# Performance work log

Measured on AMD Instinct MI355X. Metric: run time of the kernel, lower is better.

## Reference

```python
import jax, jax.numpy as jnp
import numpy as np

N = 50000      # nodes
E = 800000     # edges
D = 300        # emb_dim
G = 256        # graphs in batch
OUT = 128      # out_channels
NUM_BOND_TYPE = 6       # includes self-loop type id 4
NUM_BOND_DIR = 3
SELF_LOOP_TYPE = 4


def setup_inputs() -> dict:
    key = jax.random.key(0)
    ks = jax.random.split(key, 12)
    s = 0.05
    x = jax.random.normal(ks[0], (N, D), jnp.float32)
    edge_index = jax.random.randint(ks[1], (2, E), 0, N, dtype=jnp.int32)
    edge_attr = jax.random.randint(ks[2], (E, 2), 0, NUM_BOND_DIR, dtype=jnp.int32)
    batch = jnp.sort(jax.random.randint(ks[3], (N,), 0, G, dtype=jnp.int32))
    # 5 stacked GINConv layers: MLP(D->2D->D) + two edge-embedding tables each
    W1 = jax.random.normal(ks[4], (5, D, 2 * D), jnp.float32) * s
    b1 = jnp.zeros((5, 2 * D), jnp.float32)
    W2 = jax.random.normal(ks[5], (5, 2 * D, D), jnp.float32) * s
    b2 = jnp.zeros((5, D), jnp.float32)
    ee1 = jax.random.normal(ks[6], (5, NUM_BOND_TYPE, D), jnp.float32) * s
    ee2 = jax.random.normal(ks[7], (5, NUM_BOND_DIR, D), jnp.float32) * s
    lin1_W = jax.random.normal(ks[8], (D, D // 2), jnp.float32) * s
    lin1_b = jnp.zeros((D // 2,), jnp.float32)
    lin2_W = jax.random.normal(ks[9], (D // 2, OUT), jnp.float32) * s
    lin2_b = jnp.zeros((OUT,), jnp.float32)
    return dict(x=x, W1=W1, b1=b1, W2=W2, b2=b2, ee1=ee1, ee2=ee2,
                lin1_W=lin1_W, lin1_b=lin1_b, lin2_W=lin2_W, lin2_b=lin2_b,
                edge_index=edge_index, edge_attr=edge_attr, batch=batch)


def _gin_conv(x, edge_index, edge_attr, W1, b1, W2, b2, ee1, ee2):
    src, dst = edge_index[0], edge_index[1]
    e = ee1[edge_attr[:, 0]] + ee2[edge_attr[:, 1]]          # [E, D]
    msg = x[src] + e                                          # gather + edge-add
    agg = jax.ops.segment_sum(msg, dst, num_segments=x.shape[0])  # scatter-sum
    # self loops with edge_attr (SELF_LOOP_TYPE, 0): contributes x_i + ee1[4] + ee2[0]
    agg = agg + x + ee1[SELF_LOOP_TYPE] + ee2[0]
    h = jnp.maximum(agg @ W1 + b1, 0.0) @ W2 + b2             # MLP(D->2D->D)
    return h


def reference(x, W1, b1, W2, b2, ee1, ee2, lin1_W, lin1_b, lin2_W, lin2_b,
              edge_index, edge_attr, batch):
    h = x
    for l in range(5):
        h = _gin_conv(h, edge_index, edge_attr,
                      W1[l], b1[l], W2[l], b2[l], ee1[l], ee2[l])
    # global_add_pool over graphs
    g = jax.ops.segment_sum(h, batch, num_segments=G)          # [G, D]
    g = jnp.maximum(g @ lin1_W + lin1_b, 0.0)                  # dropout is identity in eval
    out = g @ lin2_W + lin2_b                                  # [G, OUT]
    return out
```

## Files before the change

### kernel.cpp

```cpp
#include <hip/hip_runtime.h>
#include <hip/hip_bf16.h>

#define NN 50000
#define EE 800000
#define DD 300
#define GG 256
#define RS  320
#define RSU 80

#define NK1 10
#define NT1 40
#define NK2 19
#define NT2 24
#define PACK1 ((size_t)NT1 * NK1 * 512)
#define PACK2 ((size_t)NT2 * NK2 * 512)
#define HSTR 1216

#define SCB 49

typedef short bf16x8 __attribute__((ext_vector_type(8)));
typedef float f32x4  __attribute__((ext_vector_type(4)));

__device__ inline unsigned short f2bf(float f) {
    unsigned u = __float_as_uint(f);
    return (unsigned short)((u + 0x7fffu + ((u >> 16) & 1u)) >> 16);
}
__device__ inline unsigned pk2(float a, float b) {
    return (unsigned)f2bf(a) | ((unsigned)f2bf(b) << 16);
}
__device__ inline void acc8(float* a, uint4 v) {
    a[0] += __uint_as_float(v.x << 16); a[1] += __uint_as_float(v.x & 0xffff0000u);
    a[2] += __uint_as_float(v.y << 16); a[3] += __uint_as_float(v.y & 0xffff0000u);
    a[4] += __uint_as_float(v.z << 16); a[5] += __uint_as_float(v.z & 0xffff0000u);
    a[6] += __uint_as_float(v.w << 16); a[7] += __uint_as_float(v.w & 0xffff0000u);
}
__device__ inline int deg3(int p) {
    return (p & 1023) + ((p >> 10) & 1023) + ((p >> 20) & 1023);
}

__global__ __launch_bounds__(256)
void count_kernel(const int* __restrict__ ei, const int* __restrict__ ea,
                  int* __restrict__ cnt1p, int* __restrict__ cnt2p)
{
    int e = blockIdx.x * 256 + threadIdx.x;
    if (e >= EE) return;
    int dst = ei[EE + e];
    int a0  = ea[e * 2];
    int a1  = ea[e * 2 + 1];
    atomicAdd(&cnt1p[dst], 1 << (10 * a0));
    atomicAdd(&cnt2p[dst], 1 << (10 * a1));
}

__global__ __launch_bounds__(256)
void scan1_kernel(const int* __restrict__ cnt1p, int* __restrict__ blocksum)
{
    __shared__ int ws[4];
    int tid = threadIdx.x;
    int n0 = blockIdx.x * 1024 + tid * 4;
    int s = 0;
#pragma unroll
    for (int i = 0; i < 4; ++i) {
        int n = n0 + i;
        if (n < NN) s += deg3(cnt1p[n]);
    }
    for (int off = 1; off < 64; off <<= 1) s += __shfl_xor(s, off);
    if ((tid & 63) == 0) ws[tid >> 6] = s;
    __syncthreads();
    if (tid == 0) blocksum[blockIdx.x] = ws[0] + ws[1] + ws[2] + ws[3];
}

__global__ __launch_bounds__(256)
void scan2_kernel(const int* __restrict__ cnt1p, const int* __restrict__ blocksum,
                  int* __restrict__ rowptr, int* __restrict__ cursor)
{
    __shared__ int ws[4];
    __shared__ int boff;
    int tid = threadIdx.x;
    int b   = blockIdx.x;
    if (tid < 64) {
        int v = (tid < b) ? blocksum[tid] : 0;
        for (int off = 1; off < 64; off <<= 1) v += __shfl_xor(v, off);
        if (tid == 0) boff = v;
    }
    int n0 = b * 1024 + tid * 4;
    int d[4]; int s = 0;
#pragma unroll
    for (int i = 0; i < 4; ++i) {
        int n = n0 + i;
        d[i] = (n < NN) ? deg3(cnt1p[n]) : 0;
        s += d[i];
    }
    int lane = tid & 63, w = tid >> 6;
    int inc = s;
    for (int off = 1; off < 64; off <<= 1) {
        int t = __shfl_up(inc, off);
        if (lane >= off) inc += t;
    }
    if (lane == 63) ws[w] = inc;
    __syncthreads();
    int woff = 0;
#pragma unroll
    for (int i = 0; i < 4; ++i) if (i < w) woff += ws[i];
    int excl = boff + woff + inc - s;
#pragma unroll
    for (int i = 0; i < 4; ++i) {
        int n = n0 + i;
        if (n < NN) { rowptr[n] = excl; cursor[n] = excl; }
        excl += d[i];
    }
    if (b == SCB - 1 && tid == 255) rowptr[NN] = EE;
}

__global__ __launch_bounds__(256)
void fill_kernel(const int* __restrict__ ei, int* __restrict__ cursor,
                 int* __restrict__ csr_src)
{
    int e = blockIdx.x * 256 + threadIdx.x;
    if (e >= EE) return;
    int dst = ei[EE + e];
    int src = ei[e];
    int pos = atomicAdd(&cursor[dst], 1);
    csr_src[pos] = src;
}

__global__ __launch_bounds__(256)
void pack_all(const float* __restrict__ W1, const float* __restrict__ W2,
              short* __restrict__ W1p, short* __restrict__ W2p)
{
    const int TL = NT1 * NK1 + NT2 * NK2;
    int idx = blockIdx.x * 256 + threadIdx.x;
    if (idx >= 5 * TL * 64) return;
    int lane  = idx & 63;
    int tile  = idx >> 6;
    int layer = tile / TL;
    int tl    = tile - layer * TL;
    const float* W; short* outp;
    int K, N, nt_i, kt, pos;
    if (tl < NT1 * NK1) {
        nt_i = tl / NK1; kt = tl % NK1;
        W = W1 + (size_t)layer * DD * 600;
        outp = W1p + layer * PACK1;
        K = 300; N = 600;
        pos = kt * NT1 + nt_i;
    } else {
        tl -= NT1 * NK1;
        nt_i = tl / NK2; kt = tl % NK2;
        W = W2 + (size_t)layer * 600 * DD;
        outp = W2p + layer * PACK2;
        K = 600; N = 300;
        pos = kt * NT2 + nt_i;
    }
    int col = nt_i * 16 + (lane & 15);
    int k0  = kt * 32 + (lane >> 4) * 8;
    unsigned short v[8];
#pragma unroll
    for (int j = 0; j < 8; ++j) {
        int r = k0 + j;
        float f = (r < K && col < N) ? W[(size_t)r * N + col] : 0.0f;
        v[j] = f2bf(f);
    }
    uint4 p;
    p.x = (unsigned)v[0] | ((unsigned)v[1] << 16);
    p.y = (unsigned)v[2] | ((unsigned)v[3] << 16);
    p.z = (unsigned)v[4] | ((unsigned)v[5] << 16);
    p.w = (unsigned)v[6] | ((unsigned)v[7] << 16);
    ((uint4*)outp)[(size_t)pos * 64 + lane] = p;
}

__global__ __launch_bounds__(256)
void init_kernel(const float* __restrict__ x, short* __restrict__ Xbf,
                 short* __restrict__ Ybf)
{
    int i = blockIdx.x * 256 + threadIdx.x;
    const int TX = NN * RSU;
    if (i < TX) {
        int row = i / RSU, pu = i - row * RSU;
        uint2 o = make_uint2(0u, 0u);
        if (pu < 75) {
            float4 v = ((const float4*)x)[row * 75 + pu];
            o = make_uint2(pk2(v.x, v.y), pk2(v.z, v.w));
        }
        ((uint2*)Xbf)[i] = o;
    } else {
        int j = i - TX;
        if (j < (NN + 64) * 5) {
            int row = j / 5, pu = 75 + (j - row * 5);
            ((uint2*)Ybf)[(size_t)row * RSU + pu] = make_uint2(0u, 0u);
        }
    }
}

__global__ __launch_bounds__(256)
void agg_gather(const short* __restrict__ Hbf, const int* __restrict__ rowptr,
                const int* __restrict__ csr_src, const int* __restrict__ cnt1p,
                const int* __restrict__ cnt2p, const float* __restrict__ ee1l,
                const float* __restrict__ ee2l, short* __restrict__ outbf)
{
    int n    = blockIdx.x * 4 + (threadIdx.x >> 6);
    int lane = threadIdx.x & 63;
    if (n >= NN || lane >= 40) return;
    const uint4* HU = (const uint4*)Hbf;
    const int cb = lane * 8;

    float aA[8], aB[8], aC[8], aD[8];
#pragma unroll
    for (int k = 0; k < 8; ++k) { aA[k] = 0.f; aB[k] = 0.f; aC[k] = 0.f; aD[k] = 0.f; }

    int p1 = cnt1p[n], p2 = cnt2p[n];
    float c10 = (float)(p1 & 1023), c11 = (float)((p1 >> 10) & 1023),
          c12 = (float)((p1 >> 20) & 1023);
    float c20 = (float)(p2 & 1023), c21 = (float)((p2 >> 10) & 1023),
          c22 = (float)((p2 >> 20) & 1023);

#define EEADD(rowp, s)                                                        \
    {                                                                         \
        if (lane <= 36) {                                                     \
            float4 v0 = *(const float4*)((rowp) + cb);                        \
            float4 v1 = *(const float4*)((rowp) + cb + 4);                    \
            aA[0] = fmaf(v0.x, (s), aA[0]); aA[1] = fmaf(v0.y, (s), aA[1]);   \
            aA[2] = fmaf(v0.z, (s), aA[2]); aA[3] = fmaf(v0.w, (s), aA[3]);   \
            aA[4] = fmaf(v1.x, (s), aA[4]); aA[5] = fmaf(v1.y, (s), aA[5]);   \
            aA[6] = fmaf(v1.z, (s), aA[6]); aA[7] = fmaf(v1.w, (s), aA[7]);   \
        } else if (lane == 37) {                                              \
            float4 v0 = *(const float4*)((rowp) + cb);                        \
            aA[0] = fmaf(v0.x, (s), aA[0]); aA[1] = fmaf(v0.y, (s), aA[1]);   \
            aA[2] = fmaf(v0.z, (s), aA[2]); aA[3] = fmaf(v0.w, (s), aA[3]);   \
        }                                                                     \
    }
    EEADD(ee1l + 4 * 300, 1.0f);
    EEADD(ee1l, c10); EEADD(ee1l + 300, c11); EEADD(ee1l + 600, c12);
    EEADD(ee2l, c20 + 1.0f);
    EEADD(ee2l + 300, c21); EEADD(ee2l + 600, c22);
#undef EEADD

    acc8(aB, HU[(size_t)n * 40 + lane]);

    int e   = rowptr[n];
    int end = rowptr[n + 1];
    for (; e + 4 <= end; e += 4) {
        uint4 v0 = HU[(size_t)csr_src[e]     * 40 + lane];
        uint4 v1 = HU[(size_t)csr_src[e + 1] * 40 + lane];
        uint4 v2 = HU[(size_t)csr_src[e + 2] * 40 + lane];
        uint4 v3 = HU[(size_t)csr_src[e + 3] * 40 + lane];
        acc8(aA, v0); acc8(aB, v1); acc8(aC, v2); acc8(aD, v3);
    }
    for (; e < end; ++e) acc8(aA, HU[(size_t)csr_src[e] * 40 + lane]);

    uint4 o;
    o.x = pk2(aA[0] + aB[0] + aC[0] + aD[0], aA[1] + aB[1] + aC[1] + aD[1]);
    o.y = pk2(aA[2] + aB[2] + aC[2] + aD[2], aA[3] + aB[3] + aC[3] + aD[3]);
    o.z = pk2(aA[4] + aB[4] + aC[4] + aD[4], aA[5] + aB[5] + aC[5] + aD[5]);
    o.w = pk2(aA[6] + aB[6] + aC[6] + aD[6], aA[7] + aB[7] + aC[7] + aD[7]);
    ((uint4*)(outbf + (size_t)n * RS))[lane] = o;
}

__global__ __launch_bounds__(512, 3)
void mlp_mfma(const short* __restrict__ Ybf, const short* __restrict__ W1p,
              const float* __restrict__ b1, const short* __restrict__ W2p,
              const float* __restrict__ b2, short* __restrict__ Xbf, int nrows)
{
    __shared__ __align__(16) short Hs[32 * 608];
    char* HsB = (char*)Hs;
    const int tid  = threadIdx.x;
    const int ch   = tid >> 6;
    const int lane = tid & 63;
    const int row0 = blockIdx.x * 32;
    const int l15  = lane & 15;
    const int q    = lane >> 4;
    const int hr   = q * 4;

    const short* A0 = Ybf + (size_t)(row0 + l15) * RS;
    const short* A1 = A0 + 16 * RS;
    const char* W1B = (const char*)W1p + (ch * 5) * 1024 + lane * 16;
    const char* W2B = (const char*)W2p + (ch * 3) * 1024 + lane * 16;

    f32x4 acc[5][2];
#pragma unroll
    for (int t = 0; t < 5; ++t) {
        acc[t][0] = (f32x4){0.f, 0.f, 0.f, 0.f};
        acc[t][1] = (f32x4){0.f, 0.f, 0.f, 0.f};
    }
    bf16x8 aa[3][2], bb[3][5];
#pragma unroll
    for (int p = 0; p < 2; ++p) {
        aa[p][0] = *(const bf16x8*)&A0[p * 32 + q * 8];
        aa[p][1] = *(const bf16x8*)&A1[p * 32 + q * 8];
        const char* src = W1B + p * (NT1 * 1024);
#pragma unroll
        for (int t = 0; t < 5; ++t) bb[p][t] = *(const bf16x8*)(src + t * 1024);
    }
#pragma unroll
    for (int kt = 0; kt < NK1; ++kt) {
        const int cur = kt % 3;
        if (kt + 2 < NK1) {
            const int nx = (kt + 2) % 3;
            aa[nx][0] = *(const bf16x8*)&A0[(kt + 2) * 32 + q * 8];
            aa[nx][1] = *(const bf16x8*)&A1[(kt + 2) * 32 + q * 8];
            const char* src = W1B + (kt + 2) * (NT1 * 1024);
#pragma unroll
            for (int t = 0; t < 5; ++t) bb[nx][t] = *(const bf16x8*)(src + t * 1024);
        }
#pragma unroll
        for (int t = 0; t < 5; ++t) {
            acc[t][0] = __builtin_amdgcn_mfma_f32_16x16x32_bf16(aa[cur][0], bb[cur][t], acc[t][0], 0, 0, 0);
            acc[t][1] = __builtin_amdgcn_mfma_f32_16x16x32_bf16(aa[cur][1], bb[cur][t], acc[t][1], 0, 0, 0);
        }
    }

    bf16x8 bfr[3][3];
#pragma unroll
    for (int p = 0; p < 2; ++p) {
        const char* src = W2B + p * (NT2 * 1024);
#pragma unroll
        for (int t = 0; t < 3; ++t) bfr[p][t] = *(const bf16x8*)(src + t * 1024);
    }

#pragma unroll
    for (int t = 0; t < 5; ++t) {
        int col = (ch * 5 + t) * 16 + l15;
        if (col < 608) {
            float bbv = col < 600 ? b1[col] : 0.0f;
#pragma unroll
            for (int m = 0; m < 2; ++m)
#pragma unroll
                for (int j = 0; j < 4; ++j) {
                    int row = m * 16 + hr + j;
                    float v = acc[t][m][j] + bbv;
                    v = v > 0.0f ? v : 0.0f;
                    int bo = 2 * col;
                    int boS = (bo < 1152) ? (bo ^ ((row & 7) << 4)) : bo;
                    *(short*)(HsB + row * HSTR + boS) = (short)f2bf(v);
                }
        }
    }
    __syncthreads();

    f32x4 acc2[3][2];
#pragma unroll
    for (int t = 0; t < 3; ++t) {
        acc2[t][0] = (f32x4){0.f, 0.f, 0.f, 0.f};
        acc2[t][1] = (f32x4){0.f, 0.f, 0.f, 0.f};
    }
    const int r0 = l15;
    const int r1 = r0 + 16;
    const int swz = (r0 & 7) << 4;
    bf16x8 hh[3][2];
#pragma unroll
    for (int p = 0; p < 2; ++p) {
        int bo  = p * 64 + q * 16;
        int boS = (bo < 1152) ? (bo ^ swz) : bo;
        hh[p][0] = *(const bf16x8*)(HsB + r0 * HSTR + boS);
        hh[p][1] = *(const bf16x8*)(HsB + r1 * HSTR + boS);
    }
#pragma unroll
    for (int kt = 0; kt < NK2; ++kt) {
        const int cur = kt % 3;
        if (kt + 2 < NK2) {
            const int nx = (kt + 2) % 3;
            const char* src = W2B + (kt + 2) * (NT2 * 1024);
#pragma unroll
            for (int t = 0; t < 3; ++t) bfr[nx][t] = *(const bf16x8*)(src + t * 1024);
            int bo  = (kt + 2) * 64 + q * 16;
            int boS = (bo < 1152) ? (bo ^ swz) : bo;
            hh[nx][0] = *(const bf16x8*)(HsB + r0 * HSTR + boS);
            hh[nx][1] = *(const bf16x8*)(HsB + r1 * HSTR + boS);
        }
#pragma unroll
        for (int t = 0; t < 3; ++t) {
            acc2[t][0] = __builtin_amdgcn_mfma_f32_16x16x32_bf16(hh[cur][0], bfr[cur][t], acc2[t][0], 0, 0, 0);
            acc2[t][1] = __builtin_amdgcn_mfma_f32_16x16x32_bf16(hh[cur][1], bfr[cur][t], acc2[t][1], 0, 0, 0);
        }
    }
#pragma unroll
    for (int t = 0; t < 3; ++t) {
        int col = (ch * 3 + t) * 16 + l15;
        if (col < 300) {
            float bbv = b2[col];
#pragma unroll
            for (int m = 0; m < 2; ++m)
#pragma unroll
                for (int j = 0; j < 4; ++j) {
                    int gr = row0 + m * 16 + hr + j;
                    if (gr < nrows)
                        Xbf[(size_t)gr * RS + col] = (short)f2bf(acc2[t][m][j] + bbv);
                }
        }
    }
}

__global__ __launch_bounds__(160)
void pool_kernel(const short* __restrict__ Xbf, const int* __restrict__ batch,
                 float* __restrict__ g)
{
    int tid = threadIdx.x;
    if (tid >= 150) return;
    int n0 = blockIdx.x * 64;
    int n1 = n0 + 64; if (n1 > NN) n1 = NN;
    int nlast = n1 - 1;
    float s0 = 0.0f, s1 = 0.0f;
    int cur = batch[n0];
    unsigned v = *(const unsigned*)&Xbf[(size_t)n0 * RS + tid * 2];
    for (int n = n0; n < n1; ++n) {
        int np = n + 1; np = np > nlast ? nlast : np;
        unsigned vnext = *(const unsigned*)&Xbf[(size_t)np * RS + tid * 2];
        int b = batch[n];
        if (b != cur) {
            atomicAdd(&g[cur * DD + tid * 2], s0);
            atomicAdd(&g[cur * DD + tid * 2 + 1], s1);
            s0 = 0.0f; s1 = 0.0f; cur = b;
        }
        s0 += __uint_as_float(v << 16);
        s1 += __uint_as_float(v & 0xffff0000u);
        v = vnext;
    }
    atomicAdd(&g[cur * DD + tid * 2], s0);
    atomicAdd(&g[cur * DD + tid * 2 + 1], s1);
}

__global__ __launch_bounds__(160)
void head_kernel(const float* __restrict__ g, const float* __restrict__ l1W,
                 const float* __restrict__ l1b, const float* __restrict__ l2W,
                 const float* __restrict__ l2b, float* __restrict__ out)
{
    __shared__ float g2s[152];
    int r = blockIdx.x, tid = threadIdx.x;
    const float* gr = g + r * DD;
    if (tid < 150) {
        float acc = 0.0f;
        for (int k = 0; k < DD; ++k) acc = fmaf(gr[k], l1W[k * 150 + tid], acc);
        acc += l1b[tid];
        g2s[tid] = acc > 0.0f ? acc : 0.0f;
    }
    __syncthreads();
    if (tid < 128) {
        float acc = 0.0f;
        for (int k = 0; k < 150; ++k) acc = fmaf(g2s[k], l2W[k * 128 + tid], acc);
        out[r * 128 + tid] = acc + l2b[tid];
    }
}

extern "C" void kernel_launch(void* const* d_in, const int* in_sizes, int n_in,
                              void* d_out, int out_size, void* d_ws, size_t ws_size,
                              hipStream_t stream)
{
    const float* x     = (const float*)d_in[0];
    const float* W1    = (const float*)d_in[1];
    const float* b1    = (const float*)d_in[2];
    const float* W2    = (const float*)d_in[3];
    const float* b2    = (const float*)d_in[4];
    const float* ee1   = (const float*)d_in[5];
    const float* ee2   = (const float*)d_in[6];
    const float* l1W   = (const float*)d_in[7];
    const float* l1b   = (const float*)d_in[8];
    const float* l2W   = (const float*)d_in[9];
    const float* l2b   = (const float*)d_in[10];
    const int*   ei    = (const int*)d_in[11];
    const int*   ea    = (const int*)d_in[12];
    const int*   batch = (const int*)d_in[13];
    float* out = (float*)d_out;

    short* Xbf = (short*)d_ws;
    short* Ybf = Xbf + (size_t)NN * RS;
    float* g   = (float*)(Ybf + (size_t)(NN + 64) * RS);
    short* W1p = (short*)(g + (size_t)GG * DD);
    short* W2p = W1p + 5 * PACK1;
    int* rowptr  = (int*)(W2p + 5 * PACK2);
    int* cursor  = rowptr + NN + 1;
    int* csr_src = cursor + NN;
    int* cnt1p   = csr_src + EE;
    int* cnt2p   = cnt1p + NN;
    int* blocksum = cnt2p + NN;

    hipMemsetAsync(g, 0, (size_t)GG * DD * sizeof(float), stream);
    hipMemsetAsync(cnt1p, 0, (size_t)2 * NN * sizeof(int), stream);

    count_kernel<<<(EE + 255) / 256, 256, 0, stream>>>(ei, ea, cnt1p, cnt2p);
    scan1_kernel<<<SCB, 256, 0, stream>>>(cnt1p, blocksum);
    scan2_kernel<<<SCB, 256, 0, stream>>>(cnt1p, blocksum, rowptr, cursor);
    fill_kernel<<<(EE + 255) / 256, 256, 0, stream>>>(ei, cursor, csr_src);

    {
        const int TL = NT1 * NK1 + NT2 * NK2;
        pack_all<<<(5 * TL * 64 + 255) / 256, 256, 0, stream>>>(W1, W2, W1p, W2p);
    }
    {
        int total = NN * RSU + (NN + 64) * 5;
        init_kernel<<<(total + 255) / 256, 256, 0, stream>>>(x, Xbf, Ybf);
    }

    for (int l = 0; l < 5; ++l) {
        const float* ee1l = ee1 + (size_t)l * 6 * DD;
        const float* ee2l = ee2 + (size_t)l * 3 * DD;
        agg_gather<<<(NN + 3) / 4, 256, 0, stream>>>(
            Xbf, rowptr, csr_src, cnt1p, cnt2p, ee1l, ee2l, Ybf);
        mlp_mfma<<<(NN + 31) / 32, 512, 0, stream>>>(
            Ybf, W1p + l * PACK1, b1 + (size_t)l * 600,
            W2p + l * PACK2, b2 + (size_t)l * DD, Xbf, NN);
    }
    pool_kernel<<<(NN + 63) / 64, 160, 0, stream>>>(Xbf, batch, g);
    head_kernel<<<GG, 160, 0, stream>>>(g, l1W, l1b, l2W, l2b, out);
}
```

Baseline: 1.162 ms.

## Fuse neighbor aggregation and MLP into one per-layer kernel via LDS staging

Merges the gather/aggregate kernel and the two-layer MFMA MLP into a single kernel. Each 512-thread block first aggregates its 32 rows into shared memory, then runs the MLP reading the A operand from LDS instead of global memory. Two ping-pong global buffers replace the separate intermediate buffer. This removes the intermediate write and re-read plus one launch per layer. In exchange, gather latency now sits in front of the MFMA phase inside each block, the W1 prefetch depth drops from three stages to two, and the occupancy target rises to 4, which raises register pressure.

```diff
diff --git a/kernel.cpp b/kernel.cpp
--- a/kernel.cpp
+++ b/kernel.cpp
@@ -15,6 +15,7 @@
 #define PACK1 ((size_t)NT1 * NK1 * 512)
 #define PACK2 ((size_t)NT2 * NK2 * 512)
 #define HSTR 1216
+#define ASTR 656
 
 #define SCB 49
 
@@ -190,28 +191,46 @@
     }
 }
 
-__global__ __launch_bounds__(256)
-void agg_gather(const short* __restrict__ Hbf, const int* __restrict__ rowptr,
-                const int* __restrict__ csr_src, const int* __restrict__ cnt1p,
-                const int* __restrict__ cnt2p, const float* __restrict__ ee1l,
-                const float* __restrict__ ee2l, short* __restrict__ outbf)
-{
-    int n    = blockIdx.x * 4 + (threadIdx.x >> 6);
-    int lane = threadIdx.x & 63;
-    if (n >= NN || lane >= 40) return;
-    const uint4* HU = (const uint4*)Hbf;
-    const int cb = lane * 8;
-
-    float aA[8], aB[8], aC[8], aD[8];
-#pragma unroll
-    for (int k = 0; k < 8; ++k) { aA[k] = 0.f; aB[k] = 0.f; aC[k] = 0.f; aD[k] = 0.f; }
-
-    int p1 = cnt1p[n], p2 = cnt2p[n];
-    float c10 = (float)(p1 & 1023), c11 = (float)((p1 >> 10) & 1023),
-          c12 = (float)((p1 >> 20) & 1023);
-    float c20 = (float)(p2 & 1023), c21 = (float)((p2 >> 10) & 1023),
-          c22 = (float)((p2 >> 20) & 1023);
-
+__global__ __launch_bounds__(512, 4)
+void gin_fused(const short* __restrict__ Xin, const int* __restrict__ rowptr,
+               const int* __restrict__ csr_src, const int* __restrict__ cnt1p,
+               const int* __restrict__ cnt2p, const float* __restrict__ ee1l,
+               const float* __restrict__ ee2l, const short* __restrict__ W1p,
+               const float* __restrict__ b1, const short* __restrict__ W2p,
+               const float* __restrict__ b2, short* __restrict__ Xout, int nrows)
+{
+    __shared__ __align__(16) short As[32 * 328];
+    __shared__ __align__(16) short Hs[32 * 608];
+    char* AsB = (char*)As;
+    char* HsB = (char*)Hs;
+    const int tid  = threadIdx.x;
+    const int w    = tid >> 6;
+    const int lane = tid & 63;
+    const int row0 = blockIdx.x * 32;
+    const int l15  = lane & 15;
+    const int q    = lane >> 4;
+    const int hr   = q * 4;
+
+    const char* W1B = (const char*)W1p + (w * 5) * 1024 + lane * 16;
+    const char* W2B = (const char*)W2p + (w * 3) * 1024 + lane * 16;
+
+    {
+        const uint4* HU = (const uint4*)Xin;
+        const int cb = lane * 8;
+        for (int i = 0; i < 4; ++i) {
+            int r = w * 4 + i;
+            int n = row0 + r;
+            if (lane < 40) {
+                uint4 o = make_uint4(0u, 0u, 0u, 0u);
+                if (n < nrows) {
+                    float aA[8], aB[8], aC[8], aD[8];
+#pragma unroll
+                    for (int k = 0; k < 8; ++k) { aA[k] = 0.f; aB[k] = 0.f; aC[k] = 0.f; aD[k] = 0.f; }
+                    int p1 = cnt1p[n], p2 = cnt2p[n];
+                    float c10 = (float)(p1 & 1023), c11 = (float)((p1 >> 10) & 1023),
+                          c12 = (float)((p1 >> 20) & 1023);
+                    float c20 = (float)(p2 & 1023), c21 = (float)((p2 >> 10) & 1023),
+                          c22 = (float)((p2 >> 20) & 1023);
 #define EEADD(rowp, s)                                                        \
     {                                                                         \
         if (lane <= 36) {                                                     \
@@ -227,52 +246,32 @@
             aA[2] = fmaf(v0.z, (s), aA[2]); aA[3] = fmaf(v0.w, (s), aA[3]);   \
         }                                                                     \
     }
-    EEADD(ee1l + 4 * 300, 1.0f);
-    EEADD(ee1l, c10); EEADD(ee1l + 300, c11); EEADD(ee1l + 600, c12);
-    EEADD(ee2l, c20 + 1.0f);
-    EEADD(ee2l + 300, c21); EEADD(ee2l + 600, c22);
+                    EEADD(ee1l + 4 * 300, 1.0f);
+                    EEADD(ee1l, c10); EEADD(ee1l + 300, c11); EEADD(ee1l + 600, c12);
+                    EEADD(ee2l, c20 + 1.0f);
+                    EEADD(ee2l + 300, c21); EEADD(ee2l + 600, c22);
 #undef EEADD
-
-    acc8(aB, HU[(size_t)n * 40 + lane]);
-
-    int e   = rowptr[n];
-    int end = rowptr[n + 1];
-    for (; e + 4 <= end; e += 4) {
-        uint4 v0 = HU[(size_t)csr_src[e]     * 40 + lane];
-        uint4 v1 = HU[(size_t)csr_src[e + 1] * 40 + lane];
-        uint4 v2 = HU[(size_t)csr_src[e + 2] * 40 + lane];
-        uint4 v3 = HU[(size_t)csr_src[e + 3] * 40 + lane];
-        acc8(aA, v0); acc8(aB, v1); acc8(aC, v2); acc8(aD, v3);
-    }
-    for (; e < end; ++e) acc8(aA, HU[(size_t)csr_src[e] * 40 + lane]);
-
-    uint4 o;
-    o.x = pk2(aA[0] + aB[0] + aC[0] + aD[0], aA[1] + aB[1] + aC[1] + aD[1]);
-    o.y = pk2(aA[2] + aB[2] + aC[2] + aD[2], aA[3] + aB[3] + aC[3] + aD[3]);
-    o.z = pk2(aA[4] + aB[4] + aC[4] + aD[4], aA[5] + aB[5] + aC[5] + aD[5]);
-    o.w = pk2(aA[6] + aB[6] + aC[6] + aD[6], aA[7] + aB[7] + aC[7] + aD[7]);
-    ((uint4*)(outbf + (size_t)n * RS))[lane] = o;
-}
-
-__global__ __launch_bounds__(512, 3)
-void mlp_mfma(const short* __restrict__ Ybf, const short* __restrict__ W1p,
-              const float* __restrict__ b1, const short* __restrict__ W2p,
-              const float* __restrict__ b2, short* __restrict__ Xbf, int nrows)
-{
-    __shared__ __align__(16) short Hs[32 * 608];
-    char* HsB = (char*)Hs;
-    const int tid  = threadIdx.x;
-    const int ch   = tid >> 6;
-    const int lane = tid & 63;
-    const int row0 = blockIdx.x * 32;
-    const int l15  = lane & 15;
-    const int q    = lane >> 4;
-    const int hr   = q * 4;
-
-    const short* A0 = Ybf + (size_t)(row0 + l15) * RS;
-    const short* A1 = A0 + 16 * RS;
-    const char* W1B = (const char*)W1p + (ch * 5) * 1024 + lane * 16;
-    const char* W2B = (const char*)W2p + (ch * 3) * 1024 + lane * 16;
+                    acc8(aB, HU[(size_t)n * 40 + lane]);
+                    int e   = rowptr[n];
+                    int end = rowptr[n + 1];
+                    for (; e + 4 <= end; e += 4) {
+                        uint4 v0 = HU[(size_t)csr_src[e]     * 40 + lane];
+                        uint4 v1 = HU[(size_t)csr_src[e + 1] * 40 + lane];
+                        uint4 v2 = HU[(size_t)csr_src[e + 2] * 40 + lane];
+                        uint4 v3 = HU[(size_t)csr_src[e + 3] * 40 + lane];
+                        acc8(aA, v0); acc8(aB, v1); acc8(aC, v2); acc8(aD, v3);
+                    }
+                    for (; e < end; ++e) acc8(aA, HU[(size_t)csr_src[e] * 40 + lane]);
+                    o.x = pk2(aA[0] + aB[0] + aC[0] + aD[0], aA[1] + aB[1] + aC[1] + aD[1]);
+                    o.y = pk2(aA[2] + aB[2] + aC[2] + aD[2], aA[3] + aB[3] + aC[3] + aD[3]);
+                    o.z = pk2(aA[4] + aB[4] + aC[4] + aD[4], aA[5] + aB[5] + aC[5] + aD[5]);
+                    o.w = pk2(aA[6] + aB[6] + aC[6] + aD[6], aA[7] + aB[7] + aC[7] + aD[7]);
+                }
+                *(uint4*)(AsB + r * ASTR + lane * 16) = o;
+            }
+        }
+    }
+    __syncthreads();
 
     f32x4 acc[5][2];
 #pragma unroll
@@ -280,25 +279,20 @@
         acc[t][0] = (f32x4){0.f, 0.f, 0.f, 0.f};
         acc[t][1] = (f32x4){0.f, 0.f, 0.f, 0.f};
     }
-    bf16x8 aa[3][2], bb[3][5];
-#pragma unroll
-    for (int p = 0; p < 2; ++p) {
-        aa[p][0] = *(const bf16x8*)&A0[p * 32 + q * 8];
-        aa[p][1] = *(const bf16x8*)&A1[p * 32 + q * 8];
-        const char* src = W1B + p * (NT1 * 1024);
-#pragma unroll
-        for (int t = 0; t < 5; ++t) bb[p][t] = *(const bf16x8*)(src + t * 1024);
-    }
+    bf16x8 aa[2][2], bb[2][5];
+    aa[0][0] = *(const bf16x8*)(AsB + l15 * ASTR + q * 16);
+    aa[0][1] = *(const bf16x8*)(AsB + (l15 + 16) * ASTR + q * 16);
+#pragma unroll
+    for (int t = 0; t < 5; ++t) bb[0][t] = *(const bf16x8*)(W1B + t * 1024);
 #pragma unroll
     for (int kt = 0; kt < NK1; ++kt) {
-        const int cur = kt % 3;
-        if (kt + 2 < NK1) {
-            const int nx = (kt + 2) % 3;
-            aa[nx][0] = *(const bf16x8*)&A0[(kt + 2) * 32 + q * 8];
-            aa[nx][1] = *(const bf16x8*)&A1[(kt + 2) * 32 + q * 8];
-            const char* src = W1B + (kt + 2) * (NT1 * 1024);
-#pragma unroll
-            for (int t = 0; t < 5; ++t) bb[nx][t] = *(const bf16x8*)(src + t * 1024);
+        const int cur = kt & 1, nxt = cur ^ 1;
+        if (kt < NK1 - 1) {
+            aa[nxt][0] = *(const bf16x8*)(AsB + l15 * ASTR + (kt + 1) * 64 + q * 16);
+            aa[nxt][1] = *(const bf16x8*)(AsB + (l15 + 16) * ASTR + (kt + 1) * 64 + q * 16);
+            const char* src = W1B + (kt + 1) * (NT1 * 1024);
+#pragma unroll
+            for (int t = 0; t < 5; ++t) bb[nxt][t] = *(const bf16x8*)(src + t * 1024);
         }
 #pragma unroll
         for (int t = 0; t < 5; ++t) {
@@ -317,7 +311,7 @@
 
 #pragma unroll
     for (int t = 0; t < 5; ++t) {
-        int col = (ch * 5 + t) * 16 + l15;
+        int col = (w * 5 + t) * 16 + l15;
         if (col < 608) {
             float bbv = col < 600 ? b1[col] : 0.0f;
 #pragma unroll
@@ -373,7 +367,7 @@
     }
 #pragma unroll
     for (int t = 0; t < 3; ++t) {
-        int col = (ch * 3 + t) * 16 + l15;
+        int col = (w * 3 + t) * 16 + l15;
         if (col < 300) {
             float bbv = b2[col];
 #pragma unroll
@@ -382,7 +376,7 @@
                 for (int j = 0; j < 4; ++j) {
                     int gr = row0 + m * 16 + hr + j;
                     if (gr < nrows)
-                        Xbf[(size_t)gr * RS + col] = (short)f2bf(acc2[t][m][j] + bbv);
+                        Xout[(size_t)gr * RS + col] = (short)f2bf(acc2[t][m][j] + bbv);
                 }
         }
     }
@@ -488,15 +482,17 @@
         init_kernel<<<(total + 255) / 256, 256, 0, stream>>>(x, Xbf, Ybf);
     }
 
+    short* bufA = Xbf;
+    short* bufB = Ybf;
     for (int l = 0; l < 5; ++l) {
         const float* ee1l = ee1 + (size_t)l * 6 * DD;
         const float* ee2l = ee2 + (size_t)l * 3 * DD;
-        agg_gather<<<(NN + 3) / 4, 256, 0, stream>>>(
-            Xbf, rowptr, csr_src, cnt1p, cnt2p, ee1l, ee2l, Ybf);
-        mlp_mfma<<<(NN + 31) / 32, 512, 0, stream>>>(
-            Ybf, W1p + l * PACK1, b1 + (size_t)l * 600,
-            W2p + l * PACK2, b2 + (size_t)l * DD, Xbf, NN);
-    }
-    pool_kernel<<<(NN + 63) / 64, 160, 0, stream>>>(Xbf, batch, g);
+        gin_fused<<<(NN + 31) / 32, 512, 0, stream>>>(
+            bufA, rowptr, csr_src, cnt1p, cnt2p, ee1l, ee2l,
+            W1p + l * PACK1, b1 + (size_t)l * 600,
+            W2p + l * PACK2, b2 + (size_t)l * DD, bufB, NN);
+        short* tmp = bufA; bufA = bufB; bufB = tmp;
+    }
+    pool_kernel<<<(NN + 63) / 64, 160, 0, stream>>>(bufA, batch, g);
     head_kernel<<<GG, 160, 0, stream>>>(g, l1W, l1b, l2W, l2b, out);
 }
```

Result: no change. 1.183 ms (+1.8%).
